# Performance work log

Measured on AMD Instinct MI355X. Metric: run time of the kernel, lower is better.

Reference implementation:

```python
import jax, jax.numpy as jnp
import numpy as np

TOP_K = 256
TEMP = 1.0          # max(1.0, log(0.2*256)/40) = 1.0
MARGIN = 0.1
AGE_NOISE = 8.0
EPS = 1e-12         # F.normalize eps


def _l2norm(x, axis=1):
    return x / jnp.maximum(jnp.linalg.norm(x, axis=axis, keepdims=True), EPS)


def setup_inputs() -> dict:
    key = jax.random.key(0)
    ks = jax.random.split(key, 8)
    B, A, K, M = 16, 16384, 128, 524288
    loc_preds = jax.random.normal(ks[0], (B, A, 4), jnp.float32)
    loc_targets = jax.random.normal(ks[1], (B, A, 4), jnp.float32)
    cls_preds = jax.random.normal(ks[2], (B, A, K), jnp.float32)
    cls_targets = jax.random.randint(ks[3], (B, A), 0, 21, jnp.int32)
    keys = _l2norm(jax.random.normal(ks[4], (M, K), jnp.float32))
    values = jax.random.randint(ks[5], (M,), 0, 21, jnp.int32)
    age = jax.random.uniform(ks[6], (M,), jnp.float32, minval=0.0, maxval=100.0)
    noise = jax.random.uniform(ks[7], (M,), jnp.float32)  # mapped to [-AGE_NOISE, AGE_NOISE]
    return {"loc_preds": loc_preds, "cls_preds": cls_preds,
            "loc_targets": loc_targets, "cls_targets": cls_targets,
            "keys": keys, "values": values, "age": age, "noise": noise}


def reference(loc_preds, cls_preds, loc_targets, cls_targets, keys, values, age, noise):
    M = keys.shape[0]
    B = loc_preds.shape[0]

    y = jnp.max(cls_targets, axis=1)                       # [B]
    pos = cls_targets > 0                                   # [B, A]
    num_pos = jnp.sum(pos.astype(jnp.float32), axis=1)      # [B]

    # masked smooth-l1 loc loss (sum over positive anchors, beta=1)
    diff = loc_preds - loc_targets
    ad = jnp.abs(diff)
    sl1 = jnp.where(ad < 1.0, 0.5 * diff * diff, ad - 0.5)  # [B, A, 4]
    loc_loss = jnp.sum(sl1 * pos[:, :, None]) / jnp.sum(num_pos)

    # pooled query embedding per image
    samples = jnp.sum(cls_preds * pos[:, :, None].astype(cls_preds.dtype), axis=1)
    samples = samples / num_pos[:, None]                    # [B, K]
    query = _l2norm(samples)

    # retrieval: cosine sim against memory keys + topk + softmax
    scores = jnp.matmul(query, keys.T)                      # [B, M]
    cos_sim, topk_idx = jax.lax.top_k(scores, TOP_K)        # [B, top_k]
    softmax_score = jax.nn.softmax(TEMP * cos_sim, axis=1)
    y_hat_idx = topk_idx[:, 0]                              # [B]
    y_hat = values[y_hat_idx]                               # [B]

    # memory (hinge) loss over correct / incorrect neighbors
    topk_values = values[topk_idx]                          # [B, top_k]
    correct_mask = (topk_values == y[:, None]).astype(jnp.float32)
    pos_score = jnp.max(cos_sim * correct_mask, axis=1, keepdims=True)
    neg_score = jnp.max(cos_sim * (1.0 - correct_mask), axis=1, keepdims=True)
    has_pos = (jnp.sum(correct_mask, axis=1, keepdims=True) > 0).astype(jnp.float32)
    pos_score = pos_score * has_pos
    cls_loss = jnp.mean(jnp.maximum(neg_score - pos_score + MARGIN, 0.0))

    # --- age-based memory update (non-differentiable state update) ---
    result = (y_hat == y)                                   # [B] correct predictions
    age = age + 1.0

    # correct branch: keys[idx] = normalize(keys[idx] + query); age[idx] = 0
    corr_dest = jnp.where(result, y_hat_idx, M)             # M -> dropped
    new_corr_keys = _l2norm(keys[y_hat_idx] + query)        # [B, K]
    keys = keys.at[corr_dest].set(new_corr_keys, mode='drop')
    age = age.at[corr_dest].set(0.0, mode='drop')

    # incorrect branch: evict oldest (noisy age) slots, j-th incorrect -> j-th oldest
    age_noisy = age + (noise * 2.0 - 1.0) * AGE_NOISE       # [M]
    _, oldest = jax.lax.top_k(age_noisy, B)                 # [B] oldest slots
    inc = ~result
    rank = jnp.cumsum(inc.astype(jnp.int32)) - 1            # order among incorrect
    inc_dest = jnp.where(inc, oldest[jnp.clip(rank, 0, B - 1)], M)
    keys = keys.at[inc_dest].set(query, mode='drop')
    values = values.at[inc_dest].set(y, mode='drop')
    age = age.at[inc_dest].set(0.0, mode='drop')

    return y, y_hat, softmax_score, cls_loss, loc_loss, query, keys, values, age
```

## Files before the change

### kernel.cpp

```cpp
#include <hip/hip_runtime.h>
#include <stdint.h>

typedef unsigned int u32;
typedef unsigned long long u64;

#define NB 16
#define NA 16384
#define KD 128
#define NM 524288

#define OFF_Y    0
#define OFF_YHAT 16
#define OFF_SM   32
#define OFF_CLS  4128
#define OFF_LOC  4129
#define OFF_Q    4130
#define OFF_KEYS 6178
#define OFF_VALS 67115042
#define OFF_AGE  67639330

#define WS_SAMPLES 0
#define WS_NUMPOS  8192
#define WS_YMAX    8256
#define WS_LOCSUM  8320
#define WS_QUERY   8384
#define WS_ROWLOSS 16576
#define WS_YHATIDX 16640
#define WS_RESULT  16768
#define WS_HISTS   16832
#define WS_THRESH  57792
#define WS_CANDCNT 57856
#define WS_HISTAGE 57920
#define WS_AGETH   90688
#define WS_AGECNT  90692
#define WS_AGECAND 90816
#define WS_CAND    123584
#define WS_SCORES  385728
#define WS_ZERO    123584

__global__ __launch_bounds__(256) void k_cls_sum(const float4* __restrict__ cls4,
                                                 const int* __restrict__ tgt,
                                                 float* __restrict__ samples) {
  int blk = blockIdx.x;
  int b = blk >> 5, chunk = blk & 31;
  int tid = threadIdx.x;
  int kg = tid & 31, sub = tid >> 5;
  float4 acc = make_float4(0.f, 0.f, 0.f, 0.f);
  int a0 = chunk * 512;
  for (int a = a0 + sub; a < a0 + 512; a += 8) {
    int t = tgt[b * NA + a];
    if (t > 0) {
      float4 v = cls4[((size_t)(b * NA + a)) * 32 + kg];
      acc.x += v.x; acc.y += v.y; acc.z += v.z; acc.w += v.w;
    }
  }
  __shared__ float4 red[256];
  red[tid] = acc;
  __syncthreads();
  if (tid < 32) {
    float4 s = red[tid];
    for (int r = 1; r < 8; ++r) {
      float4 v = red[r * 32 + tid];
      s.x += v.x; s.y += v.y; s.z += v.z; s.w += v.w;
    }
    atomicAdd(&samples[b * KD + kg * 4 + 0], s.x);
    atomicAdd(&samples[b * KD + kg * 4 + 1], s.y);
    atomicAdd(&samples[b * KD + kg * 4 + 2], s.z);
    atomicAdd(&samples[b * KD + kg * 4 + 3], s.w);
  }
}

__global__ __launch_bounds__(256) void k_loc(const float4* __restrict__ lp, const float4* __restrict__ lt,
                                             const int* __restrict__ tgt, float* __restrict__ numpos,
                                             int* __restrict__ ymax, float* __restrict__ locsum) {
  int i = blockIdx.x * 256 + threadIdx.x;
  int b = i >> 14;
  int t = tgt[i];
  float cnt = (t > 0) ? 1.f : 0.f;
  float sl = 0.f;
  if (t > 0) {
    float4 p = lp[i], q = lt[i];
    float d0 = p.x - q.x, d1 = p.y - q.y, d2 = p.z - q.z, d3 = p.w - q.w;
    float a0 = fabsf(d0), a1 = fabsf(d1), a2 = fabsf(d2), a3 = fabsf(d3);
    sl = ((a0 < 1.f) ? 0.5f * d0 * d0 : a0 - 0.5f)
       + ((a1 < 1.f) ? 0.5f * d1 * d1 : a1 - 0.5f)
       + ((a2 < 1.f) ? 0.5f * d2 * d2 : a2 - 0.5f)
       + ((a3 < 1.f) ? 0.5f * d3 * d3 : a3 - 0.5f);
  }
  for (int o = 32; o > 0; o >>= 1) {
    sl += __shfl_down(sl, o);
    cnt += __shfl_down(cnt, o);
    t = max(t, __shfl_down(t, o));
  }
  __shared__ float s_sl[4], s_cnt[4];
  __shared__ int s_t[4];
  int lane = threadIdx.x & 63, w = threadIdx.x >> 6;
  if (lane == 0) { s_sl[w] = sl; s_cnt[w] = cnt; s_t[w] = t; }
  __syncthreads();
  if (threadIdx.x == 0) {
    float SL = s_sl[0] + s_sl[1] + s_sl[2] + s_sl[3];
    float CN = s_cnt[0] + s_cnt[1] + s_cnt[2] + s_cnt[3];
    int T = max(max(s_t[0], s_t[1]), max(s_t[2], s_t[3]));
    atomicAdd(&numpos[b], CN);
    atomicAdd(locsum, SL);
    atomicMax(&ymax[b], T);
  }
}

__global__ __launch_bounds__(128) void k_query(const float* __restrict__ samples, const float* __restrict__ numpos,
                                               const int* __restrict__ ymax, const float* __restrict__ locsum,
                                               float* __restrict__ qws, float* __restrict__ outf) {
  int tid = threadIdx.x;
  __shared__ float partial[2];
  for (int b = 0; b < NB; ++b) {
    float np_ = numpos[b];
    float v = samples[b * KD + tid] / np_;
    float sq = v * v;
    for (int o = 32; o > 0; o >>= 1) sq += __shfl_down(sq, o);
    if ((tid & 63) == 0) partial[tid >> 6] = sq;
    __syncthreads();
    float nrm = sqrtf(partial[0] + partial[1]);
    float q = v / fmaxf(nrm, 1e-12f);
    qws[b * KD + tid] = q;
    outf[OFF_Q + b * KD + tid] = q;
    __syncthreads();
  }
  if (tid < 16) outf[OFF_Y + tid] = (float)ymax[tid];
  if (tid == 0) {
    float tot = 0.f;
    for (int b = 0; b < NB; ++b) tot += numpos[b];
    outf[OFF_LOC] = locsum[0] / tot;
  }
}

__device__ __forceinline__ float2 reduce_scatter8(const float* a, int p) {
  float t8[8];
#pragma unroll
  for (int b = 0; b < 8; ++b) {
    float keep = (p & 4) ? a[b + 8] : a[b];
    float send = (p & 4) ? a[b] : a[b + 8];
    t8[b] = keep + __shfl_xor(send, 4);
  }
  float t4[4];
#pragma unroll
  for (int b = 0; b < 4; ++b) {
    float keep = (p & 2) ? t8[b + 4] : t8[b];
    float send = (p & 2) ? t8[b] : t8[b + 4];
    t4[b] = keep + __shfl_xor(send, 2);
  }
  float t2[2];
#pragma unroll
  for (int b = 0; b < 2; ++b) {
    float keep = (p & 1) ? t4[b + 2] : t4[b];
    float send = (p & 1) ? t4[b] : t4[b + 2];
    t2[b] = keep + __shfl_xor(send, 1);
  }
  return make_float2(t2[0], t2[1]);
}

__global__ __launch_bounds__(256) void k_scores(const float4* __restrict__ keys4, const float4* __restrict__ q4,
                                                const int* __restrict__ vals, const float* __restrict__ age,
                                                float* __restrict__ outf, float* __restrict__ scores) {
  __shared__ float4 ql[512];
  __shared__ float tile[32 * 128];
  int tid = threadIdx.x;
  for (int i = tid; i < 512; i += 256) ql[i] = q4[i];
  int mc = blockIdx.x * 256 + tid;
  outf[OFF_VALS + mc] = (float)vals[mc];
  outf[OFF_AGE + mc] = age[mc] + 1.f;
  __syncthreads();

  int p = tid & 7, r = tid >> 3;
  float2* sc2 = (float2*)scores;
  int m_base = blockIdx.x * 256;

#pragma unroll 1
  for (int t = 0; t < 8; ++t) {
    int row = m_base + t * 32 + r;
    float4 kv[4];
#pragma unroll
    for (int u = 0; u < 4; ++u)
      kv[u] = keys4[(size_t)row * 32 + u * 8 + p];

    float acc[16];
#pragma unroll
    for (int b = 0; b < 16; ++b) acc[b] = 0.f;
#pragma unroll
    for (int u = 0; u < 4; ++u) {
#pragma unroll
      for (int b = 0; b < 16; ++b) {
        float4 q = ql[b * 32 + u * 8 + p];
        acc[b] += kv[u].x * q.x + kv[u].y * q.y + kv[u].z * q.z + kv[u].w * q.w;
      }
    }
    sc2[(size_t)row * 8 + p] = reduce_scatter8(acc, p);

    float4* tl4 = (float4*)(tile + r * 128);
#pragma unroll
    for (int u = 0; u < 4; ++u) tl4[u * 8 + p] = kv[u];
    __syncthreads();
    {
      size_t S = (size_t)OFF_KEYS + ((size_t)m_base + (size_t)t * 32) * KD;
      float4* dst = (float4*)(outf + S + 2);
#pragma unroll 1
      for (int j = tid; j < 1023; j += 256) {
        float4 v = make_float4(tile[j * 4 + 2], tile[j * 4 + 3],
                               tile[j * 4 + 4], tile[j * 4 + 5]);
        dst[j] = v;
      }
      if (tid == 0) {
        *(float2*)(outf + S) = make_float2(tile[0], tile[1]);
        *(float2*)(outf + S + 4094) = make_float2(tile[4094], tile[4095]);
      }
    }
    __syncthreads();
  }
}

__global__ __launch_bounds__(256) void k_hist(const float* __restrict__ scores, u32* __restrict__ ghist) {
  __shared__ u32 h[16 * 640];
  int tid = threadIdx.x;
  for (int i = tid; i < 16 * 640; i += 256) h[i] = 0;
  __syncthreads();
  int m0 = blockIdx.x * 1024;
  for (int s = 0; s < 4; ++s) {
    int m = m0 + s * 256 + tid;
    const float4* sc = (const float4*)(scores + (size_t)m * 16);
#pragma unroll
    for (int g = 0; g < 4; ++g) {
      float4 v = sc[g];
      float fv[4] = {v.x, v.y, v.z, v.w};
#pragma unroll
      for (int c = 0; c < 4; ++c) {
        float f = fv[c];
        if (f >= 0.0625f) {
          u32 u = __float_as_uint(f);
          int bin = (int)(u >> 16) - 0x3D80;
          if (bin > 639) bin = 639;
          atomicAdd(&h[(g * 4 + c) * 640 + bin], 1u);
        }
      }
    }
  }
  __syncthreads();
  for (int i = tid; i < 16 * 640; i += 256) {
    u32 v = h[i];
    if (v) atomicAdd(&ghist[i], v);
  }
}

__global__ void k_scan(const u32* __restrict__ ghist, float* __restrict__ thresh) {
  int b = blockIdx.x;
  int l = threadIdx.x;
  u32 carry = 0;
  for (int c = 0; c < 10; ++c) {
    int bin = 639 - (c * 64 + l);
    u32 v = (bin >= 0) ? ghist[b * 640 + bin] : 0u;
    u32 s = v;
    for (int o = 1; o < 64; o <<= 1) {
      u32 t = (u32)__shfl_up((int)s, o);
      if (l >= o) s += t;
    }
    u64 mask = __ballot(carry + s >= 256u);
    if (mask) {
      int first = __ffsll((long long)mask) - 1;
      if (l == first) thresh[b] = __uint_as_float(((u32)(bin + 0x3D80)) << 16);
      return;
    }
    carry += (u32)__shfl((int)s, 63);
  }
  if (l == 0) thresh[b] = __uint_as_float(((u32)0x3D80) << 16);
}

__global__ __launch_bounds__(256) void k_gather(const float* __restrict__ scores, const float* __restrict__ thresh,
                                                int* __restrict__ cnt, int2* __restrict__ cand) {
  __shared__ float th[16];
  int tid = threadIdx.x;
  if (tid < 16) th[tid] = thresh[tid];
  __syncthreads();
  int m0 = blockIdx.x * 1024;
  for (int s = 0; s < 4; ++s) {
    int m = m0 + s * 256 + tid;
    const float4* sc = (const float4*)(scores + (size_t)m * 16);
#pragma unroll
    for (int g = 0; g < 4; ++g) {
      float4 v = sc[g];
      float fv[4] = {v.x, v.y, v.z, v.w};
#pragma unroll
      for (int c = 0; c < 4; ++c) {
        int b = g * 4 + c;
        float f = fv[c];
        if (f >= th[b]) {
          int p = atomicAdd(&cnt[b], 1);
          if (p < 2048) cand[b * 2048 + p] = make_int2(__float_as_int(f), m);
        }
      }
    }
  }
}

__global__ __launch_bounds__(256) void k_topk(const int2* __restrict__ cand, const int* __restrict__ cnt,
                                              const int* __restrict__ vals, const int* __restrict__ ymax,
                                              float* __restrict__ outf, float* __restrict__ rowloss,
                                              int* __restrict__ yhatidx, int* __restrict__ result) {
  int b = blockIdx.x, tid = threadIdx.x;
  __shared__ u64 sk[2048];
  __shared__ float rb[256];
  __shared__ int sidx0;
  int nc = cnt[b];
  if (nc > 2048) nc = 2048;
  for (int i = tid; i < 2048; i += 256) {
    u64 key = 0;
    if (i < nc) {
      int2 c = cand[b * 2048 + i];
      key = ((u64)(u32)c.x << 32) | (u32)(~(u32)c.y);
    }
    sk[i] = key;
  }
  __syncthreads();
  for (int k2 = 2; k2 <= 2048; k2 <<= 1)
    for (int j2 = k2 >> 1; j2 > 0; j2 >>= 1) {
      for (int i = tid; i < 2048; i += 256) {
        int ix = i ^ j2;
        if (ix > i) {
          u64 x = sk[i], y = sk[ix];
          bool sw = ((i & k2) == 0) ? (x < y) : (x > y);
          if (sw) { sk[i] = y; sk[ix] = x; }
        }
      }
      __syncthreads();
    }
  int y = ymax[b];
  u64 kk = sk[tid];
  float c_ = __uint_as_float((u32)(kk >> 32));
  int id = (int)(~(u32)(kk & 0xFFFFFFFFull));
  id = min(max(id, 0), NM - 1);
  int vv = vals[id];
  int mk = (vv == y) ? 1 : 0;
  if (tid == 0) sidx0 = id;
  float mx = __uint_as_float((u32)(sk[0] >> 32));
  float e = expf(c_ - mx);
  rb[tid] = e; __syncthreads();
  for (int o = 128; o > 0; o >>= 1) { if (tid < o) rb[tid] += rb[tid + o]; __syncthreads(); }
  float esum = rb[0]; __syncthreads();
  outf[OFF_SM + b * 256 + tid] = e / esum;
  rb[tid] = c_ * (float)mk; __syncthreads();
  for (int o = 128; o > 0; o >>= 1) { if (tid < o) rb[tid] = fmaxf(rb[tid], rb[tid + o]); __syncthreads(); }
  float pmax = rb[0]; __syncthreads();
  rb[tid] = c_ * (float)(1 - mk); __syncthreads();
  for (int o = 128; o > 0; o >>= 1) { if (tid < o) rb[tid] = fmaxf(rb[tid], rb[tid + o]); __syncthreads(); }
  float nmax = rb[0]; __syncthreads();
  rb[tid] = (float)mk; __syncthreads();
  for (int o = 128; o > 0; o >>= 1) { if (tid < o) rb[tid] += rb[tid + o]; __syncthreads(); }
  float msum = rb[0];
  if (tid == 0) {
    float pos = (msum > 0.f) ? pmax : 0.f;
    rowloss[b] = fmaxf(nmax - pos + 0.1f, 0.f);
    int yh = vals[sidx0];
    yhatidx[b] = sidx0;
    result[b] = (yh == y) ? 1 : 0;
    outf[OFF_YHAT + b] = (float)yh;
  }
}

__global__ __launch_bounds__(128) void k_corr(const float* __restrict__ keys, const float* __restrict__ qws,
                                              const float* __restrict__ rowloss, const int* __restrict__ yhatidx,
                                              const int* __restrict__ result, float* __restrict__ outf) {
  int tid = threadIdx.x;
  __shared__ float partial[2];
  if (tid == 0) {
    float sum = 0.f;
    for (int b = 0; b < NB; ++b) sum += rowloss[b];
    outf[OFF_CLS] = sum * (1.f / 16.f);
  }
  for (int b = 0; b < NB; ++b) {
    if (result[b]) {
      int dest = yhatidx[b];
      float v = keys[(size_t)dest * KD + tid] + qws[b * KD + tid];
      float sq = v * v;
      for (int o = 32; o > 0; o >>= 1) sq += __shfl_down(sq, o);
      if ((tid & 63) == 0) partial[tid >> 6] = sq;
      __syncthreads();
      float nrm = sqrtf(partial[0] + partial[1]);
      outf[OFF_KEYS + (size_t)dest * KD + tid] = v / fmaxf(nrm, 1e-12f);
      if (tid == 0) outf[OFF_AGE + dest] = 0.f;
    }
    __syncthreads();
  }
}

__device__ __forceinline__ int age_bin(float an) {
  float x = __fmul_rn(__fadd_rn(an, 8.f), 8192.f / 120.f);
  int bin = (int)x;
  return min(max(bin, 0), 8191);
}

__global__ __launch_bounds__(256) void k_hage(const float* __restrict__ oage, const float* __restrict__ noise,
                                              u32* __restrict__ hist) {
  __shared__ u32 h[8192];
  int tid = threadIdx.x;
  for (int i = tid; i < 8192; i += 256) h[i] = 0;
  __syncthreads();
  int m0 = blockIdx.x * 4096;
  for (int s = 0; s < 16; ++s) {
    int m = m0 + s * 256 + tid;
    float an = oage[m] + (noise[m] * 2.f - 1.f) * 8.f;
    atomicAdd(&h[age_bin(an)], 1u);
  }
  __syncthreads();
  for (int i = tid; i < 8192; i += 256) {
    u32 v = h[i];
    if (v) atomicAdd(&hist[i], v);
  }
}

__global__ void k_scan_age(const u32* __restrict__ hist, int* __restrict__ T) {
  int l = threadIdx.x;
  u32 carry = 0;
  for (int c = 0; c < 128; ++c) {
    int bin = 8191 - (c * 64 + l);
    u32 v = hist[bin];
    u32 s = v;
    for (int o = 1; o < 64; o <<= 1) {
      u32 t = (u32)__shfl_up((int)s, o);
      if (l >= o) s += t;
    }
    u64 mask = __ballot(carry + s >= 16u);
    if (mask) {
      int first = __ffsll((long long)mask) - 1;
      if (l == first) *T = bin;
      return;
    }
    carry += (u32)__shfl((int)s, 63);
  }
  if (l == 0) *T = 0;
}

__global__ __launch_bounds__(256) void k_gage(const float* __restrict__ oage, const float* __restrict__ noise,
                                              const int* __restrict__ T, int* __restrict__ cnt,
                                              int2* __restrict__ cand) {
  int tb = *T;
  int tid = threadIdx.x;
  int m0 = blockIdx.x * 1024;
  for (int s = 0; s < 4; ++s) {
    int m = m0 + s * 256 + tid;
    float an = oage[m] + (noise[m] * 2.f - 1.f) * 8.f;
    if (age_bin(an) >= tb) {
      int p = atomicAdd(cnt, 1);
      if (p < 4096) {
        u32 u = __float_as_uint(an);
        u = (u & 0x80000000u) ? ~u : (u | 0x80000000u);
        cand[p] = make_int2((int)u, m);
      }
    }
  }
}

__global__ __launch_bounds__(256) void k_inc(const int* __restrict__ cnt, const int2* __restrict__ cand,
                                             const float* __restrict__ qws, const int* __restrict__ ymax,
                                             const int* __restrict__ result, float* __restrict__ outf) {
  __shared__ u64 sk[2048];
  __shared__ int oldest[16];
  __shared__ int dest[16];
  int tid = threadIdx.x;
  int nc = *cnt;
  if (nc > 2048) nc = 2048;
  for (int i = tid; i < 2048; i += 256) {
    u64 key = 0;
    if (i < nc) {
      int2 c = cand[i];
      key = ((u64)(u32)c.x << 32) | (u32)(~(u32)c.y);
    }
    sk[i] = key;
  }
  __syncthreads();
  for (int k2 = 2; k2 <= 2048; k2 <<= 1)
    for (int j2 = k2 >> 1; j2 > 0; j2 >>= 1) {
      for (int i = tid; i < 2048; i += 256) {
        int ix = i ^ j2;
        if (ix > i) {
          u64 x = sk[i], y = sk[ix];
          bool sw = ((i & k2) == 0) ? (x < y) : (x > y);
          if (sw) { sk[i] = y; sk[ix] = x; }
        }
      }
      __syncthreads();
    }
  if (tid < 16) {
    int id = (int)(~(u32)(sk[tid] & 0xFFFFFFFFull));
    oldest[tid] = min(max(id, 0), NM - 1);
  }
  __syncthreads();
  if (tid == 0) {
    int r = 0;
    for (int b = 0; b < NB; ++b) {
      if (!result[b]) { dest[b] = oldest[min(r, 15)]; r++; }
      else dest[b] = -1;
    }
  }
  __syncthreads();
  for (int b = 0; b < NB; ++b) {
    int d = dest[b];
    if (d >= 0) {
      if (tid < KD) outf[OFF_KEYS + (size_t)d * KD + tid] = qws[b * KD + tid];
      if (tid == 0) {
        outf[OFF_VALS + d] = (float)ymax[b];
        outf[OFF_AGE + d] = 0.f;
      }
    }
  }
}

extern "C" void kernel_launch(void* const* d_in, const int* in_sizes, int n_in,
                              void* d_out, int out_size, void* d_ws, size_t ws_size,
                              hipStream_t stream) {
  const float4* lp   = (const float4*)d_in[0];
  const float4* cls4 = (const float4*)d_in[1];
  const float4* lt   = (const float4*)d_in[2];
  const int* tgt     = (const int*)d_in[3];
  const float* keys  = (const float*)d_in[4];
  const int* vals    = (const int*)d_in[5];
  const float* age   = (const float*)d_in[6];
  const float* noise = (const float*)d_in[7];
  float* outf = (float*)d_out;
  char* ws = (char*)d_ws;

  hipMemsetAsync(ws, 0, WS_ZERO, stream);
  k_cls_sum<<<512, 256, 0, stream>>>(cls4, tgt, (float*)(ws + WS_SAMPLES));
  k_loc<<<1024, 256, 0, stream>>>(lp, lt, tgt, (float*)(ws + WS_NUMPOS),
                                  (int*)(ws + WS_YMAX), (float*)(ws + WS_LOCSUM));
  k_query<<<1, 128, 0, stream>>>((const float*)(ws + WS_SAMPLES), (const float*)(ws + WS_NUMPOS),
                                 (const int*)(ws + WS_YMAX), (const float*)(ws + WS_LOCSUM),
                                 (float*)(ws + WS_QUERY), outf);
  k_scores<<<2048, 256, 0, stream>>>((const float4*)keys, (const float4*)(ws + WS_QUERY),
                                     vals, age, outf, (float*)(ws + WS_SCORES));
  k_hist<<<512, 256, 0, stream>>>((const float*)(ws + WS_SCORES), (u32*)(ws + WS_HISTS));
  k_scan<<<16, 64, 0, stream>>>((const u32*)(ws + WS_HISTS), (float*)(ws + WS_THRESH));
  k_gather<<<512, 256, 0, stream>>>((const float*)(ws + WS_SCORES), (const float*)(ws + WS_THRESH),
                                    (int*)(ws + WS_CANDCNT), (int2*)(ws + WS_CAND));
  k_topk<<<16, 256, 0, stream>>>((const int2*)(ws + WS_CAND), (const int*)(ws + WS_CANDCNT),
                                 vals, (const int*)(ws + WS_YMAX), outf, (float*)(ws + WS_ROWLOSS),
                                 (int*)(ws + WS_YHATIDX), (int*)(ws + WS_RESULT));
  k_corr<<<1, 128, 0, stream>>>(keys, (const float*)(ws + WS_QUERY), (const float*)(ws + WS_ROWLOSS),
                                (const int*)(ws + WS_YHATIDX), (const int*)(ws + WS_RESULT), outf);
  k_hage<<<128, 256, 0, stream>>>(outf + OFF_AGE, noise, (u32*)(ws + WS_HISTAGE));
  k_scan_age<<<1, 64, 0, stream>>>((const u32*)(ws + WS_HISTAGE), (int*)(ws + WS_AGETH));
  k_gage<<<512, 256, 0, stream>>>(outf + OFF_AGE, noise, (const int*)(ws + WS_AGETH),
                                  (int*)(ws + WS_AGECNT), (int2*)(ws + WS_AGECAND));
  k_inc<<<1, 256, 0, stream>>>((const int*)(ws + WS_AGECNT), (const int2*)(ws + WS_AGECAND),
                               (const float*)(ws + WS_QUERY), (const int*)(ws + WS_YMAX),
                               (const int*)(ws + WS_RESULT), outf);
}
```

Measured before the change: 877.1 us.

## Merge independent kernels and reorder age-eviction ahead of top-k

```diff
diff --git a/kernel.cpp b/kernel.cpp
--- a/kernel.cpp
+++ b/kernel.cpp
@@ -36,100 +36,106 @@
 #define WS_AGECAND 90816
 #define WS_CAND    123584
 #define WS_SCORES  385728
-#define WS_ZERO    123584
-
-__global__ __launch_bounds__(256) void k_cls_sum(const float4* __restrict__ cls4,
-                                                 const int* __restrict__ tgt,
-                                                 float* __restrict__ samples) {
+#define WS_ZERO0   8384
+
+__global__ __launch_bounds__(256) void k_front(const float4* __restrict__ cls4,
+                                               const int* __restrict__ tgt,
+                                               const float4* __restrict__ lp,
+                                               const float4* __restrict__ lt,
+                                               float* __restrict__ samples,
+                                               float* __restrict__ numpos,
+                                               int* __restrict__ ymax,
+                                               float* __restrict__ locsum) {
   int blk = blockIdx.x;
-  int b = blk >> 5, chunk = blk & 31;
   int tid = threadIdx.x;
-  int kg = tid & 31, sub = tid >> 5;
-  float4 acc = make_float4(0.f, 0.f, 0.f, 0.f);
-  int a0 = chunk * 512;
-  for (int a = a0 + sub; a < a0 + 512; a += 8) {
-    int t = tgt[b * NA + a];
+  if (blk < 512) {
+    int b = blk >> 5, chunk = blk & 31;
+    int kg = tid & 31, sub = tid >> 5;
+    float4 acc = make_float4(0.f, 0.f, 0.f, 0.f);
+    int a0 = chunk * 512;
+    for (int a = a0 + sub; a < a0 + 512; a += 8) {
+      int t = tgt[b * NA + a];
+      if (t > 0) {
+        float4 v = cls4[((size_t)(b * NA + a)) * 32 + kg];
+        acc.x += v.x; acc.y += v.y; acc.z += v.z; acc.w += v.w;
+      }
+    }
+    __shared__ float4 red[256];
+    red[tid] = acc;
+    __syncthreads();
+    if (tid < 32) {
+      float4 s = red[tid];
+      for (int r = 1; r < 8; ++r) {
+        float4 v = red[r * 32 + tid];
+        s.x += v.x; s.y += v.y; s.z += v.z; s.w += v.w;
+      }
+      atomicAdd(&samples[b * KD + kg * 4 + 0], s.x);
+      atomicAdd(&samples[b * KD + kg * 4 + 1], s.y);
+      atomicAdd(&samples[b * KD + kg * 4 + 2], s.z);
+      atomicAdd(&samples[b * KD + kg * 4 + 3], s.w);
+    }
+  } else {
+    int i = (blk - 512) * 256 + tid;
+    int b = i >> 14;
+    int t = tgt[i];
+    float cnt = (t > 0) ? 1.f : 0.f;
+    float sl = 0.f;
     if (t > 0) {
-      float4 v = cls4[((size_t)(b * NA + a)) * 32 + kg];
-      acc.x += v.x; acc.y += v.y; acc.z += v.z; acc.w += v.w;
-    }
-  }
-  __shared__ float4 red[256];
-  red[tid] = acc;
+      float4 p = lp[i], q = lt[i];
+      float d0 = p.x - q.x, d1 = p.y - q.y, d2 = p.z - q.z, d3 = p.w - q.w;
+      float a0 = fabsf(d0), a1 = fabsf(d1), a2 = fabsf(d2), a3 = fabsf(d3);
+      sl = ((a0 < 1.f) ? 0.5f * d0 * d0 : a0 - 0.5f)
+         + ((a1 < 1.f) ? 0.5f * d1 * d1 : a1 - 0.5f)
+         + ((a2 < 1.f) ? 0.5f * d2 * d2 : a2 - 0.5f)
+         + ((a3 < 1.f) ? 0.5f * d3 * d3 : a3 - 0.5f);
+    }
+    for (int o = 32; o > 0; o >>= 1) {
+      sl += __shfl_down(sl, o);
+      cnt += __shfl_down(cnt, o);
+      t = max(t, __shfl_down(t, o));
+    }
+    __shared__ float s_sl[4], s_cnt[4];
+    __shared__ int s_t[4];
+    int lane = tid & 63, w = tid >> 6;
+    if (lane == 0) { s_sl[w] = sl; s_cnt[w] = cnt; s_t[w] = t; }
+    __syncthreads();
+    if (tid == 0) {
+      float SL = s_sl[0] + s_sl[1] + s_sl[2] + s_sl[3];
+      float CN = s_cnt[0] + s_cnt[1] + s_cnt[2] + s_cnt[3];
+      int T = max(max(s_t[0], s_t[1]), max(s_t[2], s_t[3]));
+      atomicAdd(&numpos[b], CN);
+      atomicAdd(locsum, SL);
+      atomicMax(&ymax[b], T);
+    }
+  }
+}
+
+__global__ __launch_bounds__(256) void k_query(const float* __restrict__ samples, const float* __restrict__ numpos,
+                                               const int* __restrict__ ymax, const float* __restrict__ locsum,
+                                               float* __restrict__ qws, float* __restrict__ outf,
+                                               u32* __restrict__ zbase) {
+  int tid = threadIdx.x, b = blockIdx.x;
+  __shared__ float part[2];
+  float v = 0.f;
+  if (tid < 128) v = samples[b * KD + tid] / numpos[b];
+  float sq = v * v;
+  for (int o = 32; o > 0; o >>= 1) sq += __shfl_down(sq, o);
+  if (tid < 128 && (tid & 63) == 0) part[tid >> 6] = sq;
   __syncthreads();
-  if (tid < 32) {
-    float4 s = red[tid];
-    for (int r = 1; r < 8; ++r) {
-      float4 v = red[r * 32 + tid];
-      s.x += v.x; s.y += v.y; s.z += v.z; s.w += v.w;
-    }
-    atomicAdd(&samples[b * KD + kg * 4 + 0], s.x);
-    atomicAdd(&samples[b * KD + kg * 4 + 1], s.y);
-    atomicAdd(&samples[b * KD + kg * 4 + 2], s.z);
-    atomicAdd(&samples[b * KD + kg * 4 + 3], s.w);
-  }
-}
-
-__global__ __launch_bounds__(256) void k_loc(const float4* __restrict__ lp, const float4* __restrict__ lt,
-                                             const int* __restrict__ tgt, float* __restrict__ numpos,
-                                             int* __restrict__ ymax, float* __restrict__ locsum) {
-  int i = blockIdx.x * 256 + threadIdx.x;
-  int b = i >> 14;
-  int t = tgt[i];
-  float cnt = (t > 0) ? 1.f : 0.f;
-  float sl = 0.f;
-  if (t > 0) {
-    float4 p = lp[i], q = lt[i];
-    float d0 = p.x - q.x, d1 = p.y - q.y, d2 = p.z - q.z, d3 = p.w - q.w;
-    float a0 = fabsf(d0), a1 = fabsf(d1), a2 = fabsf(d2), a3 = fabsf(d3);
-    sl = ((a0 < 1.f) ? 0.5f * d0 * d0 : a0 - 0.5f)
-       + ((a1 < 1.f) ? 0.5f * d1 * d1 : a1 - 0.5f)
-       + ((a2 < 1.f) ? 0.5f * d2 * d2 : a2 - 0.5f)
-       + ((a3 < 1.f) ? 0.5f * d3 * d3 : a3 - 0.5f);
-  }
-  for (int o = 32; o > 0; o >>= 1) {
-    sl += __shfl_down(sl, o);
-    cnt += __shfl_down(cnt, o);
-    t = max(t, __shfl_down(t, o));
-  }
-  __shared__ float s_sl[4], s_cnt[4];
-  __shared__ int s_t[4];
-  int lane = threadIdx.x & 63, w = threadIdx.x >> 6;
-  if (lane == 0) { s_sl[w] = sl; s_cnt[w] = cnt; s_t[w] = t; }
-  __syncthreads();
-  if (threadIdx.x == 0) {
-    float SL = s_sl[0] + s_sl[1] + s_sl[2] + s_sl[3];
-    float CN = s_cnt[0] + s_cnt[1] + s_cnt[2] + s_cnt[3];
-    int T = max(max(s_t[0], s_t[1]), max(s_t[2], s_t[3]));
-    atomicAdd(&numpos[b], CN);
-    atomicAdd(locsum, SL);
-    atomicMax(&ymax[b], T);
-  }
-}
-
-__global__ __launch_bounds__(128) void k_query(const float* __restrict__ samples, const float* __restrict__ numpos,
-                                               const int* __restrict__ ymax, const float* __restrict__ locsum,
-                                               float* __restrict__ qws, float* __restrict__ outf) {
-  int tid = threadIdx.x;
-  __shared__ float partial[2];
-  for (int b = 0; b < NB; ++b) {
-    float np_ = numpos[b];
-    float v = samples[b * KD + tid] / np_;
-    float sq = v * v;
-    for (int o = 32; o > 0; o >>= 1) sq += __shfl_down(sq, o);
-    if ((tid & 63) == 0) partial[tid >> 6] = sq;
-    __syncthreads();
-    float nrm = sqrtf(partial[0] + partial[1]);
+  if (tid < 128) {
+    float nrm = sqrtf(part[0] + part[1]);
     float q = v / fmaxf(nrm, 1e-12f);
     qws[b * KD + tid] = q;
     outf[OFF_Q + b * KD + tid] = q;
-    __syncthreads();
-  }
-  if (tid < 16) outf[OFF_Y + tid] = (float)ymax[tid];
-  if (tid == 0) {
-    float tot = 0.f;
-    for (int b = 0; b < NB; ++b) tot += numpos[b];
-    outf[OFF_LOC] = locsum[0] / tot;
+  }
+  for (int i = b * 256 + tid; i < 18466; i += 4096) zbase[i] = 0;
+  if (b == 0) {
+    if (tid < 16) outf[OFF_Y + tid] = (float)ymax[tid];
+    if (tid == 0) {
+      float tot = 0.f;
+      for (int j = 0; j < NB; ++j) tot += numpos[j];
+      outf[OFF_LOC] = locsum[0] / tot;
+    }
   }
 }
 
@@ -217,82 +223,150 @@
   }
 }
 
-__global__ __launch_bounds__(256) void k_hist(const float* __restrict__ scores, u32* __restrict__ ghist) {
+__device__ __forceinline__ int age_bin(float an) {
+  float x = __fmul_rn(__fadd_rn(an, 8.f), 8192.f / 120.f);
+  int bin = (int)x;
+  return min(max(bin, 0), 8191);
+}
+
+__global__ __launch_bounds__(256) void k_histx(const float* __restrict__ scores, u32* __restrict__ ghist,
+                                               const float* __restrict__ oage, const float* __restrict__ noise,
+                                               u32* __restrict__ ahist) {
   __shared__ u32 h[16 * 640];
+  int blk = blockIdx.x;
   int tid = threadIdx.x;
-  for (int i = tid; i < 16 * 640; i += 256) h[i] = 0;
-  __syncthreads();
-  int m0 = blockIdx.x * 1024;
-  for (int s = 0; s < 4; ++s) {
-    int m = m0 + s * 256 + tid;
-    const float4* sc = (const float4*)(scores + (size_t)m * 16);
-#pragma unroll
-    for (int g = 0; g < 4; ++g) {
-      float4 v = sc[g];
-      float fv[4] = {v.x, v.y, v.z, v.w};
-#pragma unroll
-      for (int c = 0; c < 4; ++c) {
-        float f = fv[c];
-        if (f >= 0.0625f) {
-          u32 u = __float_as_uint(f);
-          int bin = (int)(u >> 16) - 0x3D80;
-          if (bin > 639) bin = 639;
-          atomicAdd(&h[(g * 4 + c) * 640 + bin], 1u);
+  if (blk < 512) {
+    for (int i = tid; i < 16 * 640; i += 256) h[i] = 0;
+    __syncthreads();
+    int m0 = blk * 1024;
+    for (int s = 0; s < 4; ++s) {
+      int m = m0 + s * 256 + tid;
+      const float4* sc = (const float4*)(scores + (size_t)m * 16);
+#pragma unroll
+      for (int g = 0; g < 4; ++g) {
+        float4 v = sc[g];
+        float fv[4] = {v.x, v.y, v.z, v.w};
+#pragma unroll
+        for (int c = 0; c < 4; ++c) {
+          float f = fv[c];
+          if (f >= 0.0625f) {
+            u32 u = __float_as_uint(f);
+            int bin = (int)(u >> 16) - 0x3D80;
+            if (bin > 639) bin = 639;
+            atomicAdd(&h[(g * 4 + c) * 640 + bin], 1u);
+          }
         }
       }
     }
-  }
-  __syncthreads();
-  for (int i = tid; i < 16 * 640; i += 256) {
-    u32 v = h[i];
-    if (v) atomicAdd(&ghist[i], v);
-  }
-}
-
-__global__ void k_scan(const u32* __restrict__ ghist, float* __restrict__ thresh) {
-  int b = blockIdx.x;
+    __syncthreads();
+    for (int i = tid; i < 16 * 640; i += 256) {
+      u32 v = h[i];
+      if (v) atomicAdd(&ghist[i], v);
+    }
+  } else {
+    for (int i = tid; i < 8192; i += 256) h[i] = 0;
+    __syncthreads();
+    int m0 = (blk - 512) * 4096;
+    for (int s = 0; s < 16; ++s) {
+      int m = m0 + s * 256 + tid;
+      float an = oage[m] + (noise[m] * 2.f - 1.f) * 8.f;
+      atomicAdd(&h[age_bin(an)], 1u);
+    }
+    __syncthreads();
+    for (int i = tid; i < 8192; i += 256) {
+      u32 v = h[i];
+      if (v) atomicAdd(&ahist[i], v);
+    }
+  }
+}
+
+__global__ void k_scanx(const u32* __restrict__ ghist, float* __restrict__ thresh,
+                        const u32* __restrict__ ahist, int* __restrict__ T) {
+  int blk = blockIdx.x;
   int l = threadIdx.x;
-  u32 carry = 0;
-  for (int c = 0; c < 10; ++c) {
-    int bin = 639 - (c * 64 + l);
-    u32 v = (bin >= 0) ? ghist[b * 640 + bin] : 0u;
-    u32 s = v;
-    for (int o = 1; o < 64; o <<= 1) {
-      u32 t = (u32)__shfl_up((int)s, o);
-      if (l >= o) s += t;
-    }
-    u64 mask = __ballot(carry + s >= 256u);
-    if (mask) {
-      int first = __ffsll((long long)mask) - 1;
-      if (l == first) thresh[b] = __uint_as_float(((u32)(bin + 0x3D80)) << 16);
-      return;
-    }
-    carry += (u32)__shfl((int)s, 63);
-  }
-  if (l == 0) thresh[b] = __uint_as_float(((u32)0x3D80) << 16);
-}
-
-__global__ __launch_bounds__(256) void k_gather(const float* __restrict__ scores, const float* __restrict__ thresh,
-                                                int* __restrict__ cnt, int2* __restrict__ cand) {
-  __shared__ float th[16];
+  if (blk < 16) {
+    u32 carry = 0;
+    for (int c = 0; c < 10; ++c) {
+      int bin = 639 - (c * 64 + l);
+      u32 v = (bin >= 0) ? ghist[blk * 640 + bin] : 0u;
+      u32 s = v;
+      for (int o = 1; o < 64; o <<= 1) {
+        u32 t = (u32)__shfl_up((int)s, o);
+        if (l >= o) s += t;
+      }
+      u64 mask = __ballot(carry + s >= 256u);
+      if (mask) {
+        int first = __ffsll((long long)mask) - 1;
+        if (l == first) thresh[blk] = __uint_as_float(((u32)(bin + 0x3D80)) << 16);
+        return;
+      }
+      carry += (u32)__shfl((int)s, 63);
+    }
+    if (l == 0) thresh[blk] = __uint_as_float(((u32)0x3D80) << 16);
+  } else {
+    u32 carry = 0;
+    for (int c = 0; c < 128; ++c) {
+      int bin = 8191 - (c * 64 + l);
+      u32 v = ahist[bin];
+      u32 s = v;
+      for (int o = 1; o < 64; o <<= 1) {
+        u32 t = (u32)__shfl_up((int)s, o);
+        if (l >= o) s += t;
+      }
+      u64 mask = __ballot(carry + s >= 16u);
+      if (mask) {
+        int first = __ffsll((long long)mask) - 1;
+        if (l == first) *T = bin;
+        return;
+      }
+      carry += (u32)__shfl((int)s, 63);
+    }
+    if (l == 0) *T = 0;
+  }
+}
+
+__global__ __launch_bounds__(256) void k_gatherx(const float* __restrict__ scores, const float* __restrict__ thresh,
+                                                 int* __restrict__ cnt, int2* __restrict__ cand,
+                                                 const float* __restrict__ oage, const float* __restrict__ noise,
+                                                 const int* __restrict__ T, int* __restrict__ acnt,
+                                                 int2* __restrict__ acand) {
+  int blk = blockIdx.x;
   int tid = threadIdx.x;
-  if (tid < 16) th[tid] = thresh[tid];
-  __syncthreads();
-  int m0 = blockIdx.x * 1024;
-  for (int s = 0; s < 4; ++s) {
-    int m = m0 + s * 256 + tid;
-    const float4* sc = (const float4*)(scores + (size_t)m * 16);
-#pragma unroll
-    for (int g = 0; g < 4; ++g) {
-      float4 v = sc[g];
-      float fv[4] = {v.x, v.y, v.z, v.w};
-#pragma unroll
-      for (int c = 0; c < 4; ++c) {
-        int b = g * 4 + c;
-        float f = fv[c];
-        if (f >= th[b]) {
-          int p = atomicAdd(&cnt[b], 1);
-          if (p < 2048) cand[b * 2048 + p] = make_int2(__float_as_int(f), m);
+  if (blk < 512) {
+    __shared__ float th[16];
+    if (tid < 16) th[tid] = thresh[tid];
+    __syncthreads();
+    int m0 = blk * 1024;
+    for (int s = 0; s < 4; ++s) {
+      int m = m0 + s * 256 + tid;
+      const float4* sc = (const float4*)(scores + (size_t)m * 16);
+#pragma unroll
+      for (int g = 0; g < 4; ++g) {
+        float4 v = sc[g];
+        float fv[4] = {v.x, v.y, v.z, v.w};
+#pragma unroll
+        for (int c = 0; c < 4; ++c) {
+          int b = g * 4 + c;
+          float f = fv[c];
+          if (f >= th[b]) {
+            int p = atomicAdd(&cnt[b], 1);
+            if (p < 2048) cand[b * 2048 + p] = make_int2(__float_as_int(f), m);
+          }
+        }
+      }
+    }
+  } else {
+    int tb = *T;
+    int m0 = (blk - 512) * 1024;
+    for (int s = 0; s < 4; ++s) {
+      int m = m0 + s * 256 + tid;
+      float an = oage[m] + (noise[m] * 2.f - 1.f) * 8.f;
+      if (age_bin(an) >= tb) {
+        int p = atomicAdd(acnt, 1);
+        if (p < 4096) {
+          u32 u = __float_as_uint(an);
+          u = (u & 0x80000000u) ? ~u : (u | 0x80000000u);
+          acand[p] = make_int2((int)u, m);
         }
       }
     }
@@ -363,150 +437,101 @@
   }
 }
 
-__global__ __launch_bounds__(128) void k_corr(const float* __restrict__ keys, const float* __restrict__ qws,
-                                              const float* __restrict__ rowloss, const int* __restrict__ yhatidx,
-                                              const int* __restrict__ result, float* __restrict__ outf) {
+__global__ __launch_bounds__(256) void k_upd(const int* __restrict__ acnt, const int2* __restrict__ acand,
+                                             const float* __restrict__ keys, const float* __restrict__ qws,
+                                             const float* __restrict__ rowloss, const int* __restrict__ yhatidx,
+                                             const int* __restrict__ result, const int* __restrict__ ymax,
+                                             float* __restrict__ outf) {
   int tid = threadIdx.x;
-  __shared__ float partial[2];
-  if (tid == 0) {
-    float sum = 0.f;
-    for (int b = 0; b < NB; ++b) sum += rowloss[b];
-    outf[OFF_CLS] = sum * (1.f / 16.f);
-  }
-  for (int b = 0; b < NB; ++b) {
-    if (result[b]) {
-      int dest = yhatidx[b];
-      float v = keys[(size_t)dest * KD + tid] + qws[b * KD + tid];
-      float sq = v * v;
-      for (int o = 32; o > 0; o >>= 1) sq += __shfl_down(sq, o);
-      if ((tid & 63) == 0) partial[tid >> 6] = sq;
-      __syncthreads();
-      float nrm = sqrtf(partial[0] + partial[1]);
-      outf[OFF_KEYS + (size_t)dest * KD + tid] = v / fmaxf(nrm, 1e-12f);
-      if (tid == 0) outf[OFF_AGE + dest] = 0.f;
-    }
-    __syncthreads();
-  }
-}
-
-__device__ __forceinline__ int age_bin(float an) {
-  float x = __fmul_rn(__fadd_rn(an, 8.f), 8192.f / 120.f);
-  int bin = (int)x;
-  return min(max(bin, 0), 8191);
-}
-
-__global__ __launch_bounds__(256) void k_hage(const float* __restrict__ oage, const float* __restrict__ noise,
-                                              u32* __restrict__ hist) {
-  __shared__ u32 h[8192];
-  int tid = threadIdx.x;
-  for (int i = tid; i < 8192; i += 256) h[i] = 0;
-  __syncthreads();
-  int m0 = blockIdx.x * 4096;
-  for (int s = 0; s < 16; ++s) {
-    int m = m0 + s * 256 + tid;
-    float an = oage[m] + (noise[m] * 2.f - 1.f) * 8.f;
-    atomicAdd(&h[age_bin(an)], 1u);
-  }
-  __syncthreads();
-  for (int i = tid; i < 8192; i += 256) {
-    u32 v = h[i];
-    if (v) atomicAdd(&hist[i], v);
-  }
-}
-
-__global__ void k_scan_age(const u32* __restrict__ hist, int* __restrict__ T) {
-  int l = threadIdx.x;
-  u32 carry = 0;
-  for (int c = 0; c < 128; ++c) {
-    int bin = 8191 - (c * 64 + l);
-    u32 v = hist[bin];
-    u32 s = v;
-    for (int o = 1; o < 64; o <<= 1) {
-      u32 t = (u32)__shfl_up((int)s, o);
-      if (l >= o) s += t;
-    }
-    u64 mask = __ballot(carry + s >= 16u);
-    if (mask) {
-      int first = __ffsll((long long)mask) - 1;
-      if (l == first) *T = bin;
-      return;
-    }
-    carry += (u32)__shfl((int)s, 63);
-  }
-  if (l == 0) *T = 0;
-}
-
-__global__ __launch_bounds__(256) void k_gage(const float* __restrict__ oage, const float* __restrict__ noise,
-                                              const int* __restrict__ T, int* __restrict__ cnt,
-                                              int2* __restrict__ cand) {
-  int tb = *T;
-  int tid = threadIdx.x;
-  int m0 = blockIdx.x * 1024;
-  for (int s = 0; s < 4; ++s) {
-    int m = m0 + s * 256 + tid;
-    float an = oage[m] + (noise[m] * 2.f - 1.f) * 8.f;
-    if (age_bin(an) >= tb) {
-      int p = atomicAdd(cnt, 1);
-      if (p < 4096) {
-        u32 u = __float_as_uint(an);
-        u = (u & 0x80000000u) ? ~u : (u | 0x80000000u);
-        cand[p] = make_int2((int)u, m);
-      }
-    }
-  }
-}
-
-__global__ __launch_bounds__(256) void k_inc(const int* __restrict__ cnt, const int2* __restrict__ cand,
-                                             const float* __restrict__ qws, const int* __restrict__ ymax,
-                                             const int* __restrict__ result, float* __restrict__ outf) {
-  __shared__ u64 sk[2048];
-  __shared__ int oldest[16];
-  __shared__ int dest[16];
-  int tid = threadIdx.x;
-  int nc = *cnt;
+  int blk = blockIdx.x;
+  __shared__ int s_res[16], s_yhi[16], s_dinc[16], s_oldest[16];
+  __shared__ u64 s_max[4];
+  __shared__ u64 s_win;
+  __shared__ float part[4];
+  if (tid < 16) { s_res[tid] = result[tid]; s_yhi[tid] = yhatidx[tid]; }
+
+  int nc = *acnt;
   if (nc > 2048) nc = 2048;
-  for (int i = tid; i < 2048; i += 256) {
+  u64 k[8];
+#pragma unroll
+  for (int s = 0; s < 8; ++s) {
+    int i = tid + s * 256;
     u64 key = 0;
     if (i < nc) {
-      int2 c = cand[i];
+      int2 c = acand[i];
       key = ((u64)(u32)c.x << 32) | (u32)(~(u32)c.y);
     }
-    sk[i] = key;
-  }
-  __syncthreads();
-  for (int k2 = 2; k2 <= 2048; k2 <<= 1)
-    for (int j2 = k2 >> 1; j2 > 0; j2 >>= 1) {
-      for (int i = tid; i < 2048; i += 256) {
-        int ix = i ^ j2;
-        if (ix > i) {
-          u64 x = sk[i], y = sk[ix];
-          bool sw = ((i & k2) == 0) ? (x < y) : (x > y);
-          if (sw) { sk[i] = y; sk[ix] = x; }
-        }
-      }
-      __syncthreads();
-    }
-  if (tid < 16) {
-    int id = (int)(~(u32)(sk[tid] & 0xFFFFFFFFull));
-    oldest[tid] = min(max(id, 0), NM - 1);
+    k[s] = key;
+  }
+  int lane = tid & 63, wv = tid >> 6;
+  for (int r = 0; r < 16; ++r) {
+    u64 mx = k[0];
+#pragma unroll
+    for (int s = 1; s < 8; ++s) mx = (k[s] > mx) ? k[s] : mx;
+    for (int o = 32; o > 0; o >>= 1) {
+      u64 other = __shfl_down(mx, o);
+      mx = (other > mx) ? other : mx;
+    }
+    if (lane == 0) s_max[wv] = mx;
+    __syncthreads();
+    if (tid == 0) {
+      u64 w = s_max[0];
+      for (int i = 1; i < 4; ++i) w = (s_max[i] > w) ? s_max[i] : w;
+      s_win = w;
+      int id = (int)(~(u32)(w & 0xFFFFFFFFull));
+      s_oldest[r] = min(max(id, 0), NM - 1);
+    }
+    __syncthreads();
+    u64 w = s_win;
+#pragma unroll
+    for (int s = 0; s < 8; ++s) if (k[s] == w) k[s] = 0;
   }
   __syncthreads();
   if (tid == 0) {
     int r = 0;
     for (int b = 0; b < NB; ++b) {
-      if (!result[b]) { dest[b] = oldest[min(r, 15)]; r++; }
-      else dest[b] = -1;
+      if (!s_res[b]) { s_dinc[b] = s_oldest[min(r, 15)]; r++; }
+      else s_dinc[b] = -1;
     }
   }
   __syncthreads();
-  for (int b = 0; b < NB; ++b) {
-    int d = dest[b];
-    if (d >= 0) {
-      if (tid < KD) outf[OFF_KEYS + (size_t)d * KD + tid] = qws[b * KD + tid];
-      if (tid == 0) {
-        outf[OFF_VALS + d] = (float)ymax[b];
-        outf[OFF_AGE + d] = 0.f;
-      }
+
+  int b = (blk < 16) ? blk : 0;
+  int dest = s_yhi[b];
+  bool active = (blk < 16) && s_res[b];
+  if (active) {
+    for (int bp = b + 1; bp < NB; ++bp)
+      if (s_res[bp] && s_yhi[bp] == dest) active = false;
+    for (int bp = 0; bp < NB; ++bp)
+      if (s_dinc[bp] == dest) active = false;
+  }
+  float v = 0.f;
+  if (active && tid < 128) v = keys[(size_t)dest * KD + tid] + qws[b * KD + tid];
+  float sq = v * v;
+  for (int o = 32; o > 0; o >>= 1) sq += __shfl_down(sq, o);
+  if ((tid & 63) == 0) part[wv] = sq;
+  __syncthreads();
+  if (active && tid < 128) {
+    float nrm = sqrtf(part[0] + part[1]);
+    outf[OFF_KEYS + (size_t)dest * KD + tid] = v / fmaxf(nrm, 1e-12f);
+  }
+  if (active && tid == 0) outf[OFF_AGE + dest] = 0.f;
+
+  if (blk == 16) {
+    for (int bb = 0; bb < NB; ++bb) {
+      int d = s_dinc[bb];
+      if (d >= 0) {
+        if (tid < KD) outf[OFF_KEYS + (size_t)d * KD + tid] = qws[bb * KD + tid];
+        if (tid == 0) {
+          outf[OFF_VALS + d] = (float)ymax[bb];
+          outf[OFF_AGE + d] = 0.f;
+        }
+      }
+    }
+    if (tid == 0) {
+      float sum = 0.f;
+      for (int bb = 0; bb < NB; ++bb) sum += rowloss[bb];
+      outf[OFF_CLS] = sum * (1.f / 16.f);
     }
   }
 }
@@ -525,29 +550,28 @@
   float* outf = (float*)d_out;
   char* ws = (char*)d_ws;
 
-  hipMemsetAsync(ws, 0, WS_ZERO, stream);
-  k_cls_sum<<<512, 256, 0, stream>>>(cls4, tgt, (float*)(ws + WS_SAMPLES));
-  k_loc<<<1024, 256, 0, stream>>>(lp, lt, tgt, (float*)(ws + WS_NUMPOS),
-                                  (int*)(ws + WS_YMAX), (float*)(ws + WS_LOCSUM));
-  k_query<<<1, 128, 0, stream>>>((const float*)(ws + WS_SAMPLES), (const float*)(ws + WS_NUMPOS),
-                                 (const int*)(ws + WS_YMAX), (const float*)(ws + WS_LOCSUM),
-                                 (float*)(ws + WS_QUERY), outf);
+  hipMemsetAsync(ws, 0, WS_ZERO0, stream);
+  k_front<<<1536, 256, 0, stream>>>(cls4, tgt, lp, lt, (float*)(ws + WS_SAMPLES),
+                                    (float*)(ws + WS_NUMPOS), (int*)(ws + WS_YMAX),
+                                    (float*)(ws + WS_LOCSUM));
+  k_query<<<16, 256, 0, stream>>>((const float*)(ws + WS_SAMPLES), (const float*)(ws + WS_NUMPOS),
+                                  (const int*)(ws + WS_YMAX), (const float*)(ws + WS_LOCSUM),
+                                  (float*)(ws + WS_QUERY), outf, (u32*)(ws + WS_HISTS));
   k_scores<<<2048, 256, 0, stream>>>((const float4*)keys, (const float4*)(ws + WS_QUERY),
                                      vals, age, outf, (float*)(ws + WS_SCORES));
-  k_hist<<<512, 256, 0, stream>>>((const float*)(ws + WS_SCORES), (u32*)(ws + WS_HISTS));
-  k_scan<<<16, 64, 0, stream>>>((const u32*)(ws + WS_HISTS), (float*)(ws + WS_THRESH));
-  k_gather<<<512, 256, 0, stream>>>((const float*)(ws + WS_SCORES), (const float*)(ws + WS_THRESH),
-                                    (int*)(ws + WS_CANDCNT), (int2*)(ws + WS_CAND));
+  k_histx<<<640, 256, 0, stream>>>((const float*)(ws + WS_SCORES), (u32*)(ws + WS_HISTS),
+                                   outf + OFF_AGE, noise, (u32*)(ws + WS_HISTAGE));
+  k_scanx<<<17, 64, 0, stream>>>((const u32*)(ws + WS_HISTS), (float*)(ws + WS_THRESH),
+                                 (const u32*)(ws + WS_HISTAGE), (int*)(ws + WS_AGETH));
+  k_gatherx<<<1024, 256, 0, stream>>>((const float*)(ws + WS_SCORES), (const float*)(ws + WS_THRESH),
+                                      (int*)(ws + WS_CANDCNT), (int2*)(ws + WS_CAND),
+                                      outf + OFF_AGE, noise, (const int*)(ws + WS_AGETH),
+                                      (int*)(ws + WS_AGECNT), (int2*)(ws + WS_AGECAND));
   k_topk<<<16, 256, 0, stream>>>((const int2*)(ws + WS_CAND), (const int*)(ws + WS_CANDCNT),
                                  vals, (const int*)(ws + WS_YMAX), outf, (float*)(ws + WS_ROWLOSS),
                                  (int*)(ws + WS_YHATIDX), (int*)(ws + WS_RESULT));
-  k_corr<<<1, 128, 0, stream>>>(keys, (const float*)(ws + WS_QUERY), (const float*)(ws + WS_ROWLOSS),
-                                (const int*)(ws + WS_YHATIDX), (const int*)(ws + WS_RESULT), outf);
-  k_hage<<<128, 256, 0, stream>>>(outf + OFF_AGE, noise, (u32*)(ws + WS_HISTAGE));
-  k_scan_age<<<1, 64, 0, stream>>>((const u32*)(ws + WS_HISTAGE), (int*)(ws + WS_AGETH));
-  k_gage<<<512, 256, 0, stream>>>(outf + OFF_AGE, noise, (const int*)(ws + WS_AGETH),
-                                  (int*)(ws + WS_AGECNT), (int2*)(ws + WS_AGECAND));
-  k_inc<<<1, 256, 0, stream>>>((const int*)(ws + WS_AGECNT), (const int2*)(ws + WS_AGECAND),
-                               (const float*)(ws + WS_QUERY), (const int*)(ws + WS_YMAX),
-                               (const int*)(ws + WS_RESULT), outf);
-}
+  k_upd<<<17, 256, 0, stream>>>((const int*)(ws + WS_AGECNT), (const int2*)(ws + WS_AGECAND),
+                                keys, (const float*)(ws + WS_QUERY), (const float*)(ws + WS_ROWLOSS),
+                                (const int*)(ws + WS_YHATIDX), (const int*)(ws + WS_RESULT),
+                                (const int*)(ws + WS_YMAX), outf);
+}
```

Measured after the change: 791.4 us. -9.8%, faster.
